# Performance work log

Hardware: AMD Instinct MI355X
Metric: run time of the kernel (lower is better)

The kernel has to match this reference:

```python
import jax, jax.numpy as jnp
import numpy as np

B, N, D, C, Q = 8, 2048, 512, 4096, 4


def l2norm(x):
    return x / jnp.maximum(jnp.linalg.norm(x, axis=-1, keepdims=True), 1e-12)


def rotate_to(src, tgt):
    # rotation-trick transform: rotate src onto tgt, rotation detached
    sg = jax.lax.stop_gradient
    ns = jnp.linalg.norm(src, axis=-1, keepdims=True)
    nt = jnp.linalg.norm(tgt, axis=-1, keepdims=True)
    u = src / ns
    q = tgt / nt
    w = sg(l2norm(u + q))  # Householder bisector, detached
    e = src
    r = (e
         - 2.0 * jnp.sum(e * w, axis=-1, keepdims=True) * w
         + 2.0 * jnp.sum(e * sg(u), axis=-1, keepdims=True) * q)
    return r * sg(nt / ns)


def setup_inputs() -> dict:
    key = jax.random.key(0)
    k1, k2, k3 = jax.random.split(key, 3)
    x = jax.random.normal(k1, (B, N, D), jnp.float32)
    codebooks = jax.random.normal(k2, (Q, C, D), jnp.float32) * D ** -0.5
    weights = jax.random.normal(k3, (Q, D, D), jnp.float32) * D ** -0.5
    return {"x": x, "codebooks": codebooks, "weights": weights}


def reference(x, codebooks, weights):
    sg = jax.lax.stop_gradient
    num_q = codebooks.shape[0]
    residual = x
    quantized_out = jnp.zeros_like(x)
    all_idx, all_loss = [], []
    for i in range(num_q):
        implicit_cb = codebooks[i] @ weights[i].T  # Linear(dim,dim,bias=False)
        cb_n = l2norm(implicit_cb)                 # [C, D]
        x_n = l2norm(residual)                     # [B, N, D]
        # argmax of cosine similarity (no_grad in torch)
        sim = jnp.einsum('bnd,cd->bnc', sg(x_n), sg(cb_n))
        idx = jnp.argmax(sim, axis=-1)             # [B, N]
        quant = cb_n[idx]                          # [B, N, D]
        commit = (jnp.mean((sg(x_n) - quant) ** 2)
                  + 0.25 * jnp.mean((x_n - sg(quant)) ** 2))
        quant = rotate_to(x_n, quant)
        residual = residual - sg(quant)
        quantized_out = quantized_out + quant
        all_idx.append(idx)
        all_loss.append(commit)
    return quantized_out, jnp.stack(all_idx, axis=-1), jnp.stack(all_loss, axis=-1)
```

## Files before the change

kernel.cpp:

```cpp
#include <hip/hip_runtime.h>
#include <math.h>

#define RR 16384
#define DD 512
#define CC 4096
#define QQ 4
#define QOUT_SZ (RR*DD)
#define IDX_OFF QOUT_SZ
#define LOSS_OFF (QOUT_SZ + RR*QQ)
#define LOSS_COEF (1.25f / 8388608.0f)
#define NBLK_FIN (RR/4)

#define WS_RESID 0
#define WS_CBN   (RR*DD)
#define WS_RNRM  (WS_CBN + CC*DD)
#define WS_PV    (WS_RNRM + RR)
#define WS_PI    (WS_PV + RR*32*4)
#define WS_F16   (WS_PI + RR*32*4 + 4)
#define F16_A 0
#define F16_B (RR*DD)

typedef _Float16 f16x8 __attribute__((ext_vector_type(8)));
typedef short bf16x8 __attribute__((ext_vector_type(8)));
typedef float f32x4 __attribute__((ext_vector_type(4)));

__device__ __forceinline__ float waveSum(float v) {
#pragma unroll
    for (int m = 1; m < 64; m <<= 1) v += __shfl_xor(v, m, 64);
    return v;
}

template <int N>
__device__ __forceinline__ void waveSumN(float* v) {
#pragma unroll
    for (int m = 1; m < 64; m <<= 1) {
#pragma unroll
        for (int j = 0; j < N; ++j) v[j] += __shfl_xor(v[j], m, 64);
    }
}

__device__ __forceinline__ unsigned packKey(float v, int c) {
    unsigned u = __float_as_uint(v);
    u ^= (unsigned)((int)u >> 31) | 0x80000000u;
    return (u & 0xFFFFF000u) | (unsigned)(4095 - c);
}

__device__ __forceinline__ void ceDesc(unsigned &a, unsigned &b) {
    unsigned mn = a > b ? b : a;
    a = a > b ? a : b;
    b = mn;
}

__device__ __forceinline__ void merge4(unsigned k[4],
                                       unsigned b0, unsigned b1,
                                       unsigned b2, unsigned b3) {
    k[0] = k[0] > b3 ? k[0] : b3;
    k[1] = k[1] > b2 ? k[1] : b2;
    k[2] = k[2] > b1 ? k[2] : b1;
    k[3] = k[3] > b0 ? k[3] : b0;
    ceDesc(k[0], k[2]); ceDesc(k[1], k[3]);
    ceDesc(k[0], k[1]); ceDesc(k[2], k[3]);
}

__device__ __forceinline__ void merge4Shfl(unsigned k[4], int m) {
    unsigned b0 = __shfl_xor(k[0], m, 64);
    unsigned b1 = __shfl_xor(k[1], m, 64);
    unsigned b2 = __shfl_xor(k[2], m, 64);
    unsigned b3 = __shfl_xor(k[3], m, 64);
    merge4(k, b0, b1, b2, b3);
}

__device__ __forceinline__ unsigned bf16rne(float x) {
    unsigned u = __float_as_uint(x);
    return (u + 0x7FFFu + ((u >> 16) & 1u)) >> 16;
}

__global__ void initK(const float* __restrict__ x, float* __restrict__ resid) {
    int i = blockIdx.x * blockDim.x + threadIdx.x;
    int stride = gridDim.x * blockDim.x;
    for (; i < QOUT_SZ; i += stride) resid[i] = x[i];
}

__global__ void cvtSplitK(const float* __restrict__ src, short* __restrict__ hi,
                          short* __restrict__ lo, int n) {
    int i = (blockIdx.x * blockDim.x + threadIdx.x) * 4;
    int stride = gridDim.x * blockDim.x * 4;
    for (; i < n; i += stride) {
        float4 v = *(const float4*)&src[i];
        float vv[4] = {v.x, v.y, v.z, v.w};
        short hh[4], ll[4];
#pragma unroll
        for (int j = 0; j < 4; ++j) {
            unsigned hb = bf16rne(vv[j]);
            float hf = __uint_as_float(hb << 16);
            hh[j] = (short)hb;
            ll[j] = (short)bf16rne(vv[j] - hf);
        }
        *(short4*)&hi[i] = make_short4(hh[0], hh[1], hh[2], hh[3]);
        *(short4*)&lo[i] = make_short4(ll[0], ll[1], ll[2], ll[3]);
    }
}

__global__ __launch_bounds__(256)
void gemmCbMfmaK(const short* __restrict__ AHi, const short* __restrict__ ALo,
                 const short* __restrict__ BHi, const short* __restrict__ BLo,
                 float* __restrict__ out) {
    __shared__ short AH[64 * 64], AL[64 * 64];
    __shared__ short BH[64 * 64], BL[64 * 64];
    int t = threadIdx.x, w = t >> 6, lane = t & 63;
    int cBase = blockIdx.x * 64, dBase = blockIdx.y * 64;
    int mbase = (w & 1) * 32, nbase = (w >> 1) * 32;
    int l15 = lane & 15, quad = lane >> 4;

    f32x4 acc[2][2];
#pragma unroll
    for (int i = 0; i < 2; ++i)
#pragma unroll
        for (int j = 0; j < 2; ++j) acc[i][j] = (f32x4){0.f, 0.f, 0.f, 0.f};

    int rsub = lane >> 3;
    int swz = (lane & 7) ^ rsub;

    for (int k0 = 0; k0 < DD; k0 += 64) {
        __syncthreads();
#pragma unroll
        for (int j = 0; j < 2; ++j) {
            int r0 = j * 32 + 8 * w;
            __builtin_amdgcn_global_load_lds(
                (const __attribute__((address_space(1))) void*)&AHi[(size_t)(cBase + r0 + rsub) * DD + k0 + swz * 8],
                (__attribute__((address_space(3))) void*)&AH[r0 * 64], 16, 0, 0);
            __builtin_amdgcn_global_load_lds(
                (const __attribute__((address_space(1))) void*)&ALo[(size_t)(cBase + r0 + rsub) * DD + k0 + swz * 8],
                (__attribute__((address_space(3))) void*)&AL[r0 * 64], 16, 0, 0);
            __builtin_amdgcn_global_load_lds(
                (const __attribute__((address_space(1))) void*)&BHi[(size_t)(dBase + r0 + rsub) * DD + k0 + swz * 8],
                (__attribute__((address_space(3))) void*)&BH[r0 * 64], 16, 0, 0);
            __builtin_amdgcn_global_load_lds(
                (const __attribute__((address_space(1))) void*)&BLo[(size_t)(dBase + r0 + rsub) * DD + k0 + swz * 8],
                (__attribute__((address_space(3))) void*)&BL[r0 * 64], 16, 0, 0);
        }
        __syncthreads();
#pragma unroll
        for (int kh = 0; kh < 2; ++kh) {
            int chunk = (kh * 4 + quad) ^ (l15 & 7);
            bf16x8 ah[2], al[2], bh[2], bl[2];
#pragma unroll
            for (int tm = 0; tm < 2; ++tm) {
                ah[tm] = *(const bf16x8*)&AH[(mbase + tm * 16 + l15) * 64 + chunk * 8];
                al[tm] = *(const bf16x8*)&AL[(mbase + tm * 16 + l15) * 64 + chunk * 8];
            }
#pragma unroll
            for (int tn = 0; tn < 2; ++tn) {
                bh[tn] = *(const bf16x8*)&BH[(nbase + tn * 16 + l15) * 64 + chunk * 8];
                bl[tn] = *(const bf16x8*)&BL[(nbase + tn * 16 + l15) * 64 + chunk * 8];
            }
#pragma unroll
            for (int tn = 0; tn < 2; ++tn)
#pragma unroll
                for (int tm = 0; tm < 2; ++tm) {
                    acc[tm][tn] = __builtin_amdgcn_mfma_f32_16x16x32_bf16(
                        ah[tm], bh[tn], acc[tm][tn], 0, 0, 0);
                    acc[tm][tn] = __builtin_amdgcn_mfma_f32_16x16x32_bf16(
                        ah[tm], bl[tn], acc[tm][tn], 0, 0, 0);
                    acc[tm][tn] = __builtin_amdgcn_mfma_f32_16x16x32_bf16(
                        al[tm], bh[tn], acc[tm][tn], 0, 0, 0);
                }
        }
    }

#pragma unroll
    for (int tm = 0; tm < 2; ++tm)
#pragma unroll
        for (int tn = 0; tn < 2; ++tn)
#pragma unroll
            for (int r = 0; r < 4; ++r) {
                int row = cBase + mbase + tm * 16 + quad * 4 + r;
                int col = dBase + nbase + tn * 16 + l15;
                out[(size_t)row * DD + col] = acc[tm][tn][r];
            }
}

__global__ void rowNormCvtK(float* __restrict__ buf, _Float16* __restrict__ bf16) {
    int wave = threadIdx.x >> 6, lane = threadIdx.x & 63;
    int row = blockIdx.x * 4 + wave;
    float* p = buf + (size_t)row * DD;
    float4 v0 = *(float4*)&p[lane * 8];
    float4 v1 = *(float4*)&p[lane * 8 + 4];
    float ss = v0.x*v0.x + v0.y*v0.y + v0.z*v0.z + v0.w*v0.w
             + v1.x*v1.x + v1.y*v1.y + v1.z*v1.z + v1.w*v1.w;
    ss = waveSum(ss);
    float nrm = fmaxf(sqrtf(ss), 1e-12f);
    float vals[8] = {v0.x/nrm, v0.y/nrm, v0.z/nrm, v0.w/nrm,
                     v1.x/nrm, v1.y/nrm, v1.z/nrm, v1.w/nrm};
    *(float4*)&p[lane * 8]     = make_float4(vals[0], vals[1], vals[2], vals[3]);
    *(float4*)&p[lane * 8 + 4] = make_float4(vals[4], vals[5], vals[6], vals[7]);
    f16x8 hv;
#pragma unroll
    for (int j = 0; j < 8; ++j) hv[j] = (_Float16)vals[j];
    *(f16x8*)&bf16[(size_t)row * DD + lane * 8] = hv;
}

__global__ void residCvtK(const float* __restrict__ resid,
                          float* __restrict__ rnrm, _Float16* __restrict__ af16) {
    int wave = threadIdx.x >> 6, lane = threadIdx.x & 63;
    int row = blockIdx.x * 4 + wave;
    const float* p = resid + (size_t)row * DD;
    float4 v0 = *(const float4*)&p[lane * 8];
    float4 v1 = *(const float4*)&p[lane * 8 + 4];
    float vals[8] = {v0.x, v0.y, v0.z, v0.w, v1.x, v1.y, v1.z, v1.w};
    float ss = 0.f;
#pragma unroll
    for (int j = 0; j < 8; ++j) ss += vals[j] * vals[j];
    ss = waveSum(ss);
    if (lane == 0) rnrm[row] = fmaxf(sqrtf(ss), 1e-12f);
    f16x8 hv;
#pragma unroll
    for (int j = 0; j < 8; ++j) hv[j] = (_Float16)vals[j];
    *(f16x8*)&af16[(size_t)row * DD + lane * 8] = hv;
}

__global__ __launch_bounds__(512)
void simMfmaK(
    const _Float16* __restrict__ Af16, const _Float16* __restrict__ Bf16,
    unsigned* __restrict__ pk) {
    __shared__ _Float16 Alds[128 * 64];
    __shared__ _Float16 Blds[128 * 64];
    int t = threadIdx.x, w = t >> 6, lane = t & 63;
    int rowBase = blockIdx.x * 128;
    int cBase = blockIdx.y * 128;
    int mbase = (w & 3) * 32, nbase = (w >> 2) * 64;
    int l15 = lane & 15, quad = lane >> 4;

    f32x4 acc[2][4];
#pragma unroll
    for (int i = 0; i < 2; ++i)
#pragma unroll
        for (int j = 0; j < 4; ++j) acc[i][j] = (f32x4){0.f, 0.f, 0.f, 0.f};

    int rsub = lane >> 3;
    int swz = (lane & 7) ^ rsub;

    for (int k0 = 0; k0 < DD; k0 += 64) {
        __syncthreads();
#pragma unroll
        for (int j = 0; j < 2; ++j) {
            int rA = rowBase + j * 64 + 8 * w + rsub;
            int rB = cBase + j * 64 + 8 * w + rsub;
            __builtin_amdgcn_global_load_lds(
                (const __attribute__((address_space(1))) void*)&Af16[(size_t)rA * DD + k0 + swz * 8],
                (__attribute__((address_space(3))) void*)&Alds[(j * 64 + 8 * w) * 64], 16, 0, 0);
            __builtin_amdgcn_global_load_lds(
                (const __attribute__((address_space(1))) void*)&Bf16[(size_t)rB * DD + k0 + swz * 8],
                (__attribute__((address_space(3))) void*)&Blds[(j * 64 + 8 * w) * 64], 16, 0, 0);
        }
        __syncthreads();
#pragma unroll
        for (int kh = 0; kh < 2; ++kh) {
            int chunk = (kh * 4 + quad) ^ (l15 & 7);
            f16x8 af[2];
#pragma unroll
            for (int tm = 0; tm < 2; ++tm)
                af[tm] = *(const f16x8*)&Alds[(mbase + tm * 16 + l15) * 64 + chunk * 8];
#pragma unroll
            for (int tn = 0; tn < 4; ++tn) {
                f16x8 bf = *(const f16x8*)&Blds[(nbase + tn * 16 + l15) * 64 + chunk * 8];
#pragma unroll
                for (int tm = 0; tm < 2; ++tm)
                    acc[tm][tn] = __builtin_amdgcn_mfma_f32_16x16x32_f16(
                        af[tm], bf, acc[tm][tn], 0, 0, 0);
            }
        }
    }

    int gkey = (cBase >> 6) + (w >> 2);
#pragma unroll
    for (int tm = 0; tm < 2; ++tm) {
#pragma unroll
        for (int r = 0; r < 4; ++r) {
            unsigned t0 = packKey(acc[tm][0][r], cBase + nbase + 0 * 16 + l15);
            unsigned t1 = packKey(acc[tm][1][r], cBase + nbase + 1 * 16 + l15);
            unsigned t2 = packKey(acc[tm][2][r], cBase + nbase + 2 * 16 + l15);
            unsigned t3 = packKey(acc[tm][3][r], cBase + nbase + 3 * 16 + l15);
            ceDesc(t0, t1); ceDesc(t2, t3);
            unsigned k0 = t0 > t2 ? t0 : t2;
            unsigned mn = t0 > t2 ? t2 : t0;
            unsigned mx = t1 > t3 ? t1 : t3;
            unsigned k1 = mn > mx ? mn : mx;
#pragma unroll
            for (int m = 1; m < 16; m <<= 1) {
                unsigned b0 = __shfl_xor(k0, m, 64);
                unsigned b1 = __shfl_xor(k1, m, 64);
                unsigned m0 = k0 > b0 ? k0 : b0;
                unsigned n0 = k0 > b0 ? b0 : k0;
                unsigned m1 = k1 > b1 ? k1 : b1;
                k0 = m0;
                k1 = n0 > m1 ? n0 : m1;
            }
            if (l15 == 0) {
                int rowg = rowBase + mbase + tm * 16 + quad * 4 + r;
                *(uint2*)&pk[(size_t)rowg * 128 + gkey * 2] = make_uint2(k0, k1);
            }
        }
    }
}

__global__ void finalizeK(float* __restrict__ resid,
                          float* __restrict__ rnrm,
                          const float* __restrict__ cbn,
                          const unsigned* __restrict__ pk,
                          float* __restrict__ dout,
                          float* __restrict__ lossPart,
                          _Float16* __restrict__ af16, int q) {
    __shared__ float sL[4];
    int wave = threadIdx.x >> 6, lane = threadIdx.x & 63;
    int row = blockIdx.x * 4 + wave;
    float* xr = resid + (size_t)row * DD;
    float nrm = rnrm[row];
    float4 a0 = *(float4*)&xr[lane * 8];
    float4 a1 = *(float4*)&xr[lane * 8 + 4];
    float orig[8] = {a0.x,a0.y,a0.z,a0.w,a1.x,a1.y,a1.z,a1.w};
    float x[8];
#pragma unroll
    for (int j = 0; j < 8; ++j) x[j] = orig[j] / nrm;

    uint2 kp = *(const uint2*)&pk[(size_t)row * 128 + lane * 2];
    unsigned k[4] = {kp.x, kp.y, 0u, 0u};
#pragma unroll
    for (int m = 1; m < 64; m <<= 1) merge4Shfl(k, m);
    int cand[4];
#pragma unroll
    for (int j = 0; j < 4; ++j)
        cand[j] = 4095 - (int)(__shfl(k[j], 0, 64) & 0xFFFu);

    float cv[4][8];
#pragma unroll
    for (int j = 0; j < 4; ++j) {
        const float* cbj = cbn + (size_t)cand[j] * DD;
        float4 c0 = *(const float4*)&cbj[lane * 8];
        float4 c1 = *(const float4*)&cbj[lane * 8 + 4];
        cv[j][0]=c0.x; cv[j][1]=c0.y; cv[j][2]=c0.z; cv[j][3]=c0.w;
        cv[j][4]=c1.x; cv[j][5]=c1.y; cv[j][6]=c1.z; cv[j][7]=c1.w;
    }
    float s[4];
#pragma unroll
    for (int j = 0; j < 4; ++j) {
        float acc = 0.f;
#pragma unroll
        for (int e = 0; e < 8; ++e) acc += x[e] * cv[j][e];
        s[j] = acc;
    }
    waveSumN<4>(s);
    float sBest = -3e38f; int idx = 0x7fffffff, sel = 0;
#pragma unroll
    for (int j = 0; j < 4; ++j) {
        if (s[j] > sBest || (s[j] == sBest && cand[j] < idx)) {
            sBest = s[j]; idx = cand[j]; sel = j;
        }
    }

    float qv[8];
#pragma unroll
    for (int e = 0; e < 8; ++e)
        qv[e] = sel == 0 ? cv[0][e] : sel == 1 ? cv[1][e]
              : sel == 2 ? cv[2][e] : cv[3][e];

    float red3[3] = {0.f, 0.f, 0.f};
#pragma unroll
    for (int j = 0; j < 8; ++j) {
        red3[0] += x[j] * x[j];
        red3[1] += qv[j] * qv[j];
        float d = x[j] - qv[j];
        red3[2] += d * d;
    }
    waveSumN<3>(red3);
    float ns = sqrtf(red3[0]), nt = sqrtf(red3[1]), lrow = red3[2];

    float u[8], qn[8], wv[8];
    float nw2 = 0.f;
#pragma unroll
    for (int j = 0; j < 8; ++j) {
        u[j] = x[j] / ns;
        qn[j] = qv[j] / nt;
        wv[j] = u[j] + qn[j];
        nw2 += wv[j] * wv[j];
    }
    nw2 = waveSum(nw2);
    float nw = fmaxf(sqrtf(nw2), 1e-12f);
    float red2[2] = {0.f, 0.f};
#pragma unroll
    for (int j = 0; j < 8; ++j) {
        wv[j] = wv[j] / nw;
        red2[0] += x[j] * wv[j];
        red2[1] += x[j] * u[j];
    }
    waveSumN<2>(red2);
    float dew = red2[0], deu = red2[1];
    float scale = nt / ns;

    float r[8], nres[8];
    float ss = 0.f;
#pragma unroll
    for (int j = 0; j < 8; ++j) {
        r[j] = (x[j] - 2.0f * dew * wv[j] + 2.0f * deu * qn[j]) * scale;
        nres[j] = orig[j] - r[j];
        ss += nres[j] * nres[j];
    }

    *(float4*)&xr[lane * 8]     = make_float4(nres[0], nres[1], nres[2], nres[3]);
    *(float4*)&xr[lane * 8 + 4] = make_float4(nres[4], nres[5], nres[6], nres[7]);
    ss = waveSum(ss);
    if (lane == 0) rnrm[row] = fmaxf(sqrtf(ss), 1e-12f);
    f16x8 hv;
#pragma unroll
    for (int j = 0; j < 8; ++j) hv[j] = (_Float16)nres[j];
    *(f16x8*)&af16[(size_t)row * DD + lane * 8] = hv;

    if (lane == 0) {
        dout[IDX_OFF + row * 4 + q] = (float)idx;
        sL[wave] = lrow;
    }
    __syncthreads();
    if (threadIdx.x == 0) {
        lossPart[(size_t)q * NBLK_FIN + blockIdx.x] =
            (sL[0] + sL[1] + sL[2] + sL[3]) * LOSS_COEF;
    }
}

__global__ void qoutK(const float* __restrict__ x, const float* __restrict__ resid,
                      float* __restrict__ dout) {
    int i = blockIdx.x * blockDim.x + threadIdx.x;
    int stride = gridDim.x * blockDim.x;
    for (; i < QOUT_SZ; i += stride) dout[i] = x[i] - resid[i];
}

__global__ void lossWriteK(const float* __restrict__ lossPart,
                           float* __restrict__ dout) {
    int q = threadIdx.x >> 6, lane = threadIdx.x & 63;
    float s = 0.f;
    for (int i = lane; i < NBLK_FIN; i += 64)
        s += lossPart[(size_t)q * NBLK_FIN + i];
    s = waveSum(s);
    if (lane == 0) dout[LOSS_OFF + q] = s;
}

extern "C" void kernel_launch(void* const* d_in, const int* in_sizes, int n_in,
                              void* d_out, int out_size, void* d_ws, size_t ws_size,
                              hipStream_t stream) {
    const float* x = (const float*)d_in[0];
    const float* codebooks = (const float*)d_in[1];
    const float* weights = (const float*)d_in[2];
    float* dout = (float*)d_out;
    float* w = (float*)d_ws;

    float* resid = w + WS_RESID;
    float* cbn   = w + WS_CBN;
    float* rnrm  = w + WS_RNRM;
    unsigned* pk = (unsigned*)(w + WS_PV);
    float* lossPart = w + WS_PI;
    _Float16* f16base = (_Float16*)(w + WS_F16);
    _Float16* Af16 = f16base + F16_A;
    _Float16* Bf16 = f16base + F16_B;
    short* cbHi = (short*)(w + WS_PV);
    short* cbLo = cbHi + (size_t)CC * DD;
    short* wHi  = (short*)(w + WS_PI + 32768);
    short* wLo  = wHi + (size_t)DD * DD;

    initK<<<2048, 256, 0, stream>>>(x, resid);
    residCvtK<<<RR / 4, 256, 0, stream>>>(resid, rnrm, Af16);

    for (int q = 0; q < QQ; ++q) {
        cvtSplitK<<<512, 256, 0, stream>>>(codebooks + (size_t)q * CC * DD,
                                           cbHi, cbLo, CC * DD);
        cvtSplitK<<<128, 256, 0, stream>>>(weights + (size_t)q * DD * DD,
                                           wHi, wLo, DD * DD);
        gemmCbMfmaK<<<dim3(CC / 64, DD / 64), 256, 0, stream>>>(
            cbHi, cbLo, wHi, wLo, cbn);
        rowNormCvtK<<<CC / 4, 256, 0, stream>>>(cbn, Bf16);
        simMfmaK<<<dim3(RR / 128, CC / 128), 512, 0, stream>>>(Af16, Bf16, pk);
        finalizeK<<<RR / 4, 256, 0, stream>>>(resid, rnrm, cbn, pk,
                                              dout, lossPart, Af16, q);
    }
    qoutK<<<2048, 256, 0, stream>>>(x, resid, dout);
    lossWriteK<<<1, 256, 0, stream>>>(lossPart, dout);
}
```

Before: 778.4 us.

## Double-buffer LDS tiles in similarity MFMA kernel to overlap loads with compute

Splits the A and B shared-memory tiles into two buffers. The global-to-LDS loads for the next K-step are issued before the MFMAs on the current buffer, with explicit vmcnt waits and barriers in place of the earlier sync-load-sync pattern. The aim is to hide global load latency behind MFMA work. This doubles LDS use per block to 64KB, which may reduce occupancy, and it depends on hand-tuned waitcnt values being correct.

```diff
diff --git a/kernel.cpp b/kernel.cpp
--- a/kernel.cpp
+++ b/kernel.cpp
@@ -223,8 +223,8 @@
 void simMfmaK(
     const _Float16* __restrict__ Af16, const _Float16* __restrict__ Bf16,
     unsigned* __restrict__ pk) {
-    __shared__ _Float16 Alds[128 * 64];
-    __shared__ _Float16 Blds[128 * 64];
+    __shared__ _Float16 Alds[2][128 * 64];
+    __shared__ _Float16 Blds[2][128 * 64];
     int t = threadIdx.x, w = t >> 6, lane = t & 63;
     int rowBase = blockIdx.x * 128;
     int cBase = blockIdx.y * 128;
@@ -240,37 +240,56 @@
     int rsub = lane >> 3;
     int swz = (lane & 7) ^ rsub;
 
-    for (int k0 = 0; k0 < DD; k0 += 64) {
-        __syncthreads();
-#pragma unroll
-        for (int j = 0; j < 2; ++j) {
-            int rA = rowBase + j * 64 + 8 * w + rsub;
-            int rB = cBase + j * 64 + 8 * w + rsub;
-            __builtin_amdgcn_global_load_lds(
-                (const __attribute__((address_space(1))) void*)&Af16[(size_t)rA * DD + k0 + swz * 8],
-                (__attribute__((address_space(3))) void*)&Alds[(j * 64 + 8 * w) * 64], 16, 0, 0);
-            __builtin_amdgcn_global_load_lds(
-                (const __attribute__((address_space(1))) void*)&Bf16[(size_t)rB * DD + k0 + swz * 8],
-                (__attribute__((address_space(3))) void*)&Blds[(j * 64 + 8 * w) * 64], 16, 0, 0);
-        }
-        __syncthreads();
+#define SIM_STAGE(b, tt)                                                          \
+    {                                                                             \
+        int k0s = (tt) * 64;                                                      \
+        _Pragma("unroll")                                                         \
+        for (int j = 0; j < 2; ++j) {                                             \
+            int rA = rowBase + j * 64 + 8 * w + rsub;                             \
+            int rB = cBase + j * 64 + 8 * w + rsub;                               \
+            __builtin_amdgcn_global_load_lds(                                     \
+                (const __attribute__((address_space(1))) void*)&Af16[(size_t)rA * DD + k0s + swz * 8], \
+                (__attribute__((address_space(3))) void*)&Alds[b][(j * 64 + 8 * w) * 64], 16, 0, 0);   \
+            __builtin_amdgcn_global_load_lds(                                     \
+                (const __attribute__((address_space(1))) void*)&Bf16[(size_t)rB * DD + k0s + swz * 8], \
+                (__attribute__((address_space(3))) void*)&Blds[b][(j * 64 + 8 * w) * 64], 16, 0, 0);   \
+        }                                                                         \
+    }
+
+    SIM_STAGE(0, 0);
+
+#pragma unroll
+    for (int tt = 0; tt < 8; ++tt) {
+        int buf = tt & 1;
+        if (tt < 7) {
+            SIM_STAGE(buf ^ 1, tt + 1);
+            asm volatile("s_waitcnt vmcnt(4)" ::: "memory");
+        } else {
+            asm volatile("s_waitcnt vmcnt(0)" ::: "memory");
+        }
+        __builtin_amdgcn_s_barrier();
+        __builtin_amdgcn_sched_barrier(0);
 #pragma unroll
         for (int kh = 0; kh < 2; ++kh) {
             int chunk = (kh * 4 + quad) ^ (l15 & 7);
             f16x8 af[2];
 #pragma unroll
             for (int tm = 0; tm < 2; ++tm)
-                af[tm] = *(const f16x8*)&Alds[(mbase + tm * 16 + l15) * 64 + chunk * 8];
+                af[tm] = *(const f16x8*)&Alds[buf][(mbase + tm * 16 + l15) * 64 + chunk * 8];
 #pragma unroll
             for (int tn = 0; tn < 4; ++tn) {
-                f16x8 bf = *(const f16x8*)&Blds[(nbase + tn * 16 + l15) * 64 + chunk * 8];
+                f16x8 bf = *(const f16x8*)&Blds[buf][(nbase + tn * 16 + l15) * 64 + chunk * 8];
 #pragma unroll
                 for (int tm = 0; tm < 2; ++tm)
                     acc[tm][tn] = __builtin_amdgcn_mfma_f32_16x16x32_f16(
                         af[tm], bf, acc[tm][tn], 0, 0, 0);
             }
         }
-    }
+        __builtin_amdgcn_sched_barrier(0);
+        asm volatile("" ::: "memory");
+        __builtin_amdgcn_s_barrier();
+    }
+#undef SIM_STAGE
 
     int gkey = (cBase >> 6) + (w >> 2);
 #pragma unroll
```

New measurement: 773.7 us. Within noise of the previous version (-0.6%).
